# Kernel tuning notes

Hardware: AMD Instinct MI355X
Metric: run time of the kernel (lower is better)

The kernel has to match this reference:

```python
import jax, jax.numpy as jnp
import numpy as np

# torch grid_sample semantics: grid[...,0] indexes width, grid[...,1] height, grid[...,2] depth;
# align_corners=True -> idx = (g+1)/2*(size-1); padding_mode='zeros' -> out-of-range taps contribute 0.

def _bilinear(plane, gx, gy):
    # plane: (C,H,W); gx,gy: (P,) in [-1,1]. Returns (P,C).
    C, H, W = plane.shape
    ix = (gx + 1.0) * 0.5 * (W - 1)
    iy = (gy + 1.0) * 0.5 * (H - 1)
    x0 = jnp.floor(ix); y0 = jnp.floor(iy)
    wx = ix - x0; wy = iy - y0
    x0i = x0.astype(jnp.int32); x1i = x0i + 1
    y0i = y0.astype(jnp.int32); y1i = y0i + 1
    def tap(xi, yi):
        valid = ((xi >= 0) & (xi < W) & (yi >= 0) & (yi < H)).astype(plane.dtype)
        v = plane[:, jnp.clip(yi, 0, H - 1), jnp.clip(xi, 0, W - 1)]  # (C,P)
        return v * valid
    out = (tap(x0i, y0i) * ((1 - wx) * (1 - wy)) + tap(x1i, y0i) * (wx * (1 - wy))
         + tap(x0i, y1i) * ((1 - wx) * wy)      + tap(x1i, y1i) * (wx * wy))
    return out.T  # (P,C)


def _trilinear(vol, gx, gy, gz):
    # vol: (C,D,H,W); gx->W, gy->H, gz->D. Returns (P,C).
    C, D, H, W = vol.shape
    ix = (gx + 1.0) * 0.5 * (W - 1)
    iy = (gy + 1.0) * 0.5 * (H - 1)
    iz = (gz + 1.0) * 0.5 * (D - 1)
    x0 = jnp.floor(ix); y0 = jnp.floor(iy); z0 = jnp.floor(iz)
    wx = ix - x0; wy = iy - y0; wz = iz - z0
    x0i = x0.astype(jnp.int32); y0i = y0.astype(jnp.int32); z0i = z0.astype(jnp.int32)
    def tap(xi, yi, zi):
        valid = ((xi >= 0) & (xi < W) & (yi >= 0) & (yi < H) & (zi >= 0) & (zi < D)).astype(vol.dtype)
        v = vol[:, jnp.clip(zi, 0, D - 1), jnp.clip(yi, 0, H - 1), jnp.clip(xi, 0, W - 1)]
        return v * valid
    out = jnp.zeros((C, gx.shape[0]), vol.dtype)
    for dz, wz_ in ((0, 1 - wz), (1, wz)):
        for dy, wy_ in ((0, 1 - wy), (1, wy)):
            for dx, wx_ in ((0, 1 - wx), (1, wx)):
                out = out + tap(x0i + dx, y0i + dy, z0i + dz) * (wx_ * wy_ * wz_)
    return out.T


def setup_inputs() -> dict:
    key = jax.random.key(0)
    ks = jax.random.split(key, 16)
    P, Cp, Np_, Cl, Nl, Cv, Nv = 262144, 32, 128, 64, 128, 16, 64
    s = 0.001
    d = {
        'coordinates': jax.random.uniform(ks[0], (1, P, 3), jnp.float32, -1.0, 1.0),
        'plane_xy': jax.random.normal(ks[1], (Cp, Np_, Np_)) * s,
        'plane_yz': jax.random.normal(ks[2], (Cp, Np_, Np_)) * s,
        'plane_xz': jax.random.normal(ks[3], (Cp, Np_, Np_)) * s,
        'plane_xy_g': jax.random.normal(ks[4], (Cp, Np_, Np_)) * s,
        'plane_yz_g': jax.random.normal(ks[5], (Cp, Np_, Np_)) * s,
        'plane_xz_g': jax.random.normal(ks[6], (Cp, Np_, Np_)) * s,
        'line_x': jax.random.normal(ks[7], (Cl, Nl, 1)) * s,
        'line_y': jax.random.normal(ks[8], (Cl, Nl, 1)) * s,
        'line_z': jax.random.normal(ks[9], (Cl, Nl, 1)) * s,
        'line_x_g': jax.random.normal(ks[10], (Cl, Nl, 1)) * s,
        'line_y_g': jax.random.normal(ks[11], (Cl, Nl, 1)) * s,
        'line_z_g': jax.random.normal(ks[12], (Cl, Nl, 1)) * s,
        'volume': jax.random.normal(ks[13], (Cv, Nv, Nv, Nv)) * s,
        'volume_g': jax.random.normal(ks[14], (Cv, Nv, Nv, Nv)) * s,
    }
    return d


def reference(coordinates, plane_xy, plane_yz, plane_xz, plane_xy_g, plane_yz_g, plane_xz_g,
              line_x, line_y, line_z, line_x_g, line_y_g, line_z_g, volume, volume_g):
    c = coordinates[0]  # (P,3), batch squeezed as in torch .squeeze(0)
    x, y, z = c[:, 0], c[:, 1], c[:, 2]
    zero = jnp.zeros_like(x)
    # Planes: coords2d (a,b) -> grid x=a (width), grid y=b (height).
    xy_e = _bilinear(plane_xy, x, y); xy_g = _bilinear(plane_xy_g, x, y)
    yz_e = _bilinear(plane_yz, y, z); yz_g = _bilinear(plane_yz_g, y, z)
    xz_e = _bilinear(plane_xz, x, z); xz_g = _bilinear(plane_xz_g, x, z)
    feats = jnp.sum(xy_e * (xy_g >= 0) + yz_e * (yz_g >= 0) + xz_e * (xz_g >= 0), axis=-1)
    # Lines: grid pair is (coord, 0) -> coord indexes the singleton width dim (faithful to torch).
    x_e = _bilinear(line_x, x, zero); x_g = _bilinear(line_x_g, x, zero)
    y_e = _bilinear(line_y, y, zero); y_g = _bilinear(line_y_g, y, zero)
    z_e = _bilinear(line_z, z, zero); z_g = _bilinear(line_z_g, z, zero)
    line_feats = jnp.sum(x_e * (x_g >= 0) + y_e * (y_g >= 0) + z_e * (z_g >= 0), axis=-1)
    # Volume: grid (x,y,z) -> x:W, y:H, z:D.
    v_e = _trilinear(volume, x, y, z); v_g = _trilinear(volume_g, x, y, z)
    vol_feats = jnp.sum(v_e * (v_g >= 0), axis=-1)
    return feats + line_feats + vol_feats  # (P,)
```

## Files before the change

kernel.cpp:

```cpp
#include <hip/hip_runtime.h>
#include <hip/hip_bf16.h>

#pragma clang fp contract(off)

typedef unsigned short u16;
typedef unsigned int u32;
typedef __attribute__((ext_vector_type(4))) float f32x4;
typedef __attribute__((ext_vector_type(8))) unsigned short u16x8;
typedef __attribute__((ext_vector_type(4))) unsigned short u16x4;

__device__ __forceinline__ float bf2f(u16 u) {
    union { unsigned int i; float f; } v; v.i = ((unsigned int)u) << 16; return v.f;
}
__device__ __forceinline__ u16 f2bf(float f) {
    __hip_bfloat16 h = __float2bfloat16(f);
    return *(u16*)&h;
}

__device__ __forceinline__ int cell_of(float x, float y, float z)
{
    int cx = (int)fminf(fmaxf((x + 1.0f) * 4.0f, 0.0f), 7.0f);
    int cy = (int)fminf(fmaxf((y + 1.0f) * 4.0f, 0.0f), 7.0f);
    int cz = (int)fminf(fmaxf((z + 1.0f) * 4.0f, 0.0f), 7.0f);
    return cx + (cy << 3) + (cz << 6);
}

__global__ __launch_bounds__(256) void fused_prep_count(
    const float* __restrict__ pxy, const float* __restrict__ pxyg,
    const float* __restrict__ pyz, const float* __restrict__ pyzg,
    const float* __restrict__ pxz, const float* __restrict__ pxzg,
    const float* __restrict__ vol, const float* __restrict__ volg,
    char* __restrict__ tpxy, char* __restrict__ tpyz, char* __restrict__ tpxz,
    char* __restrict__ tv,
    const float* __restrict__ coords, u32* __restrict__ hist, int P)
{
    __shared__ float smem[4352];
    const int b = blockIdx.x;
    const int t = threadIdx.x;

    if (b < 768) {
        int which = b >> 8, blk = b & 255;
        const float* e = (which == 0) ? pxy  : (which == 1) ? pyz  : pxz;
        const float* g = (which == 0) ? pxyg : (which == 1) ? pyzg : pxzg;
        char* dst      = (which == 0) ? tpxy : (which == 1) ? tpyz : tpxz;
        const int tbase = blk * 64;
#pragma unroll
        for (int i = 0; i < 4; ++i) {
            int eidx = i * 256 + t;
            int c = eidx >> 4;
            int q = eidx & 15;
            const float* src = (c < 32) ? e : g;
            int cs = (c < 32) ? c : (c - 32);
            f32x4 v = *(const f32x4*)(src + (size_t)cs * 16384 + tbase + q * 4);
            *(f32x4*)&smem[c * 68 + q * 4] = v;
        }
        __syncthreads();
#pragma unroll
        for (int i = 0; i < 3; ++i) {
            int sid = i * 256 + t;
            int rec = sid / 12;
            int seg = sid % 12;
            char* outp = dst + (size_t)(tbase + rec) * 192 + seg * 16;
            if (seg < 4) {
                u16x8 pk;
#pragma unroll
                for (int k = 0; k < 8; ++k) pk[k] = f2bf(smem[(seg * 8 + k) * 68 + rec]);
                *(u16x8*)outp = pk;
            } else {
                f32x4 pk;
#pragma unroll
                for (int k = 0; k < 4; ++k) pk[k] = smem[(32 + (seg - 4) * 4 + k) * 68 + rec];
                *(f32x4*)outp = pk;
            }
        }
    } else if (b < 2816) {
        int blk = b - 768;
        const int tbase = blk * 128;
#pragma unroll
        for (int i = 0; i < 4; ++i) {
            int eidx = i * 256 + t;
            int c = eidx >> 5;
            int q = eidx & 31;
            const float* src = (c < 16) ? vol : volg;
            int cs = (c < 16) ? c : (c - 16);
            f32x4 v = *(const f32x4*)(src + (size_t)cs * 262144 + tbase + q * 4);
            *(f32x4*)&smem[c * 132 + q * 4] = v;
        }
        __syncthreads();
#pragma unroll
        for (int i = 0; i < 3; ++i) {
            int sid = i * 256 + t;
            int rec = sid / 6;
            int seg = sid % 6;
            char* outp = tv + (size_t)(tbase + rec) * 96 + seg * 16;
            if (seg < 2) {
                u16x8 pk;
#pragma unroll
                for (int k = 0; k < 8; ++k) pk[k] = f2bf(smem[(seg * 8 + k) * 132 + rec]);
                *(u16x8*)outp = pk;
            } else {
                f32x4 pk;
#pragma unroll
                for (int k = 0; k < 4; ++k) pk[k] = smem[(16 + (seg - 2) * 4 + k) * 132 + rec];
                *(f32x4*)outp = pk;
            }
        }
    } else {
        u32* h = (u32*)smem;
        int blk = b - 2816;
        h[t] = 0u; h[t + 256] = 0u;
        __syncthreads();
        int p = blk * 256 + t;
        if (p < P) {
            float x = coords[3 * p + 0];
            float y = coords[3 * p + 1];
            float z = coords[3 * p + 2];
            atomicAdd(&h[cell_of(x, y, z)], 1u);
        }
        __syncthreads();
        u32* hb = hist + (size_t)blk * 512;
        hb[t] = h[t];
        hb[t + 256] = h[t + 256];
    }
}

__global__ __launch_bounds__(256) void cell_base(
    const u32* __restrict__ hist, u32* __restrict__ base,
    u32* __restrict__ totals, int nb)
{
    int c = blockIdx.x;
    int t = threadIdx.x;
    int b0 = t * 4;
    u32 v[4];
#pragma unroll
    for (int i = 0; i < 4; ++i)
        v[i] = (b0 + i < nb) ? hist[(size_t)(b0 + i) * 512 + c] : 0u;
    u32 lsum = v[0] + v[1] + v[2] + v[3];
    __shared__ u32 ls[256];
    ls[t] = lsum;
    __syncthreads();
#pragma unroll
    for (int off = 1; off < 256; off <<= 1) {
        u32 x = (t >= off) ? ls[t - off] : 0u;
        __syncthreads();
        ls[t] += x;
        __syncthreads();
    }
    u32 acc = ls[t] - lsum;
#pragma unroll
    for (int i = 0; i < 4; ++i) {
        if (b0 + i < nb) base[(size_t)(b0 + i) * 512 + c] = acc;
        acc += v[i];
    }
    if (t == 255) totals[c] = acc;
}

__global__ __launch_bounds__(256) void bucket_scatter2(
    const float* __restrict__ coords, const u32* __restrict__ base,
    const u32* __restrict__ totals, u32* __restrict__ perm, int P)
{
    __shared__ u32 lh[512];
    __shared__ u32 ts[512];
    __shared__ u32 torig[512];
    int t = threadIdx.x;
    lh[t] = 0u; lh[t + 256] = 0u;
    u32 a0 = totals[t], a1 = totals[t + 256];
    ts[t] = a0; ts[t + 256] = a1;
    torig[t] = a0; torig[t + 256] = a1;
    __syncthreads();
#pragma unroll
    for (int off = 1; off < 512; off <<= 1) {
        u32 x0 = (t >= off) ? ts[t - off] : 0u;
        u32 x1 = (t + 256 >= off) ? ts[t + 256 - off] : 0u;
        __syncthreads();
        ts[t] += x0; ts[t + 256] += x1;
        __syncthreads();
    }
    ts[t]       -= torig[t];
    ts[t + 256] -= torig[t + 256];
    __syncthreads();

    int p = blockIdx.x * 256 + t;
    if (p < P) {
        float x = coords[3 * p + 0];
        float y = coords[3 * p + 1];
        float z = coords[3 * p + 2];
        int cell = cell_of(x, y, z);
        u32 rank = atomicAdd(&lh[cell], 1u);
        u32 pos = ts[cell] + base[(size_t)blockIdx.x * 512 + cell] + rank;
        perm[pos] = (u32)p;
    }
}

__device__ __forceinline__ float plane_lane(
    const char* __restrict__ tp, float gx, float gy, int s)
{
    float ix = fminf(fmaxf((gx + 1.0f) * 0.5f * 127.0f, 0.0f), 127.0f);
    float iy = fminf(fmaxf((gy + 1.0f) * 0.5f * 127.0f, 0.0f), 127.0f);
    float x0f = floorf(ix), y0f = floorf(iy);
    float wx = ix - x0f, wy = iy - y0f;
    int x0 = (int)x0f, y0 = (int)y0f;
    int x1 = x0 + 1, y1 = y0 + 1;
    float vx1 = (x1 < 128) ? 1.0f : 0.0f;
    float vy1 = (y1 < 128) ? 1.0f : 0.0f;
    int x1c = min(x1, 127), y1c = min(y1, 127);
    float omwx = 1.0f - wx, omwy = 1.0f - wy;
    float ws4[4];
    ws4[0] = omwx * omwy;
    ws4[1] = (wx * omwy) * vx1;
    ws4[2] = (omwx * wy) * vy1;
    ws4[3] = ((wx * wy) * vx1) * vy1;
    unsigned o[4];
    o[0] = (unsigned)(y0  * 128 + x0 ) * 192u;
    o[1] = (unsigned)(y0  * 128 + x1c) * 192u;
    o[2] = (unsigned)(y1c * 128 + x0 ) * 192u;
    o[3] = (unsigned)(y1c * 128 + x1c) * 192u;

    const int eoff = s * 16;
    const int goff = 64 + s * 32;
    f32x4 ea0 = {0.0f, 0.0f, 0.0f, 0.0f}, ea1 = {0.0f, 0.0f, 0.0f, 0.0f};
    f32x4 ga0 = {0.0f, 0.0f, 0.0f, 0.0f}, ga1 = {0.0f, 0.0f, 0.0f, 0.0f};
#pragma unroll
    for (int t = 0; t < 4; ++t) {
        const char* bp = tp + o[t];
        float w = ws4[t];
        u16x8 ev = *(const u16x8*)(bp + eoff);
        f32x4 g0 = *(const f32x4*)(bp + goff);
        f32x4 g1 = *(const f32x4*)(bp + goff + 16);
#pragma unroll
        for (int j = 0; j < 4; ++j) {
            ga0[j] = ga0[j] + g0[j] * w;
            ga1[j] = ga1[j] + g1[j] * w;
            ea0[j] = fmaf(bf2f(ev[j]), w, ea0[j]);
            ea1[j] = fmaf(bf2f(ev[j + 4]), w, ea1[j]);
        }
    }
    float acc = 0.0f;
#pragma unroll
    for (int j = 0; j < 4; ++j) {
        acc += (ga0[j] >= 0.0f) ? ea0[j] : 0.0f;
        acc += (ga1[j] >= 0.0f) ? ea1[j] : 0.0f;
    }
    return acc;
}

__device__ __forceinline__ float vol_lane(
    const char* __restrict__ tv, float gx, float gy, float gz, int s)
{
    float ix = fminf(fmaxf((gx + 1.0f) * 0.5f * 63.0f, 0.0f), 63.0f);
    float iy = fminf(fmaxf((gy + 1.0f) * 0.5f * 63.0f, 0.0f), 63.0f);
    float iz = fminf(fmaxf((gz + 1.0f) * 0.5f * 63.0f, 0.0f), 63.0f);
    float x0f = floorf(ix), y0f = floorf(iy), z0f = floorf(iz);
    float wx = ix - x0f, wy = iy - y0f, wz = iz - z0f;
    int x0 = (int)x0f, y0 = (int)y0f, z0 = (int)z0f;
    int x1 = x0 + 1, y1 = y0 + 1, z1 = z0 + 1;
    float fx[2] = {1.0f - wx, wx}, fy[2] = {1.0f - wy, wy}, fz[2] = {1.0f - wz, wz};
    float vx[2] = {1.0f, (x1 < 64) ? 1.0f : 0.0f};
    float vy[2] = {1.0f, (y1 < 64) ? 1.0f : 0.0f};
    float vz[2] = {1.0f, (z1 < 64) ? 1.0f : 0.0f};
    int xi[2] = {x0, min(x1, 63)}, yi[2] = {y0, min(y1, 63)}, zi[2] = {z0, min(z1, 63)};

    unsigned off[8];
    float w[8];
#pragma unroll
    for (int dz = 0; dz < 2; ++dz)
#pragma unroll
        for (int dy = 0; dy < 2; ++dy)
#pragma unroll
            for (int dx = 0; dx < 2; ++dx) {
                int tt = (dz << 2) | (dy << 1) | dx;
                w[tt] = (((fx[dx] * fy[dy]) * fz[dz]) * vx[dx]) * (vy[dy] * vz[dz]);
                off[tt] = (unsigned)((zi[dz] * 64 + yi[dy]) * 64 + xi[dx]) * 96u;
            }
    const int eoff = s * 8;
    const int goff = 32 + s * 16;
    f32x4 ea = {0.0f, 0.0f, 0.0f, 0.0f}, ga = {0.0f, 0.0f, 0.0f, 0.0f};
#pragma unroll
    for (int tt = 0; tt < 8; ++tt) {
        const char* bp = tv + off[tt];
        float wt = w[tt];
        u16x4 ev = *(const u16x4*)(bp + eoff);
        f32x4 gv = *(const f32x4*)(bp + goff);
#pragma unroll
        for (int j = 0; j < 4; ++j) {
            ga[j] = ga[j] + gv[j] * wt;
            ea[j] = fmaf(bf2f(ev[j]), wt, ea[j]);
        }
    }
    float acc = 0.0f;
#pragma unroll
    for (int j = 0; j < 4; ++j)
        acc += (ga[j] >= 0.0f) ? ea[j] : 0.0f;
    return acc;
}

__device__ __forceinline__ float line_pair(const float* __restrict__ e,
                                           const float* __restrict__ g, int c)
{
    float ev = e[c * 128 + 63] * 0.5f + e[c * 128 + 64] * 0.5f;
    float gv = g[c * 128 + 63] * 0.5f + g[c * 128 + 64] * 0.5f;
    return (gv >= 0.0f) ? ev : 0.0f;
}

__device__ __forceinline__ float block_line_const(
    const float* lx, const float* ly, const float* lz,
    const float* lxg, const float* lyg, const float* lzg)
{
    __shared__ float lc_sh;
    int t = threadIdx.x;
    if (t < 64) {
        float part = line_pair(lx, lxg, t) + line_pair(ly, lyg, t) + line_pair(lz, lzg, t);
#pragma unroll
        for (int off = 32; off > 0; off >>= 1) part += __shfl_down(part, off);
        if (t == 0) lc_sh = part;
    }
    __syncthreads();
    return lc_sh;
}

__global__ __launch_bounds__(256) void ctri_main_L2(
    const float* __restrict__ coords, const u32* __restrict__ perm,
    const float* __restrict__ lx,  const float* __restrict__ ly,  const float* __restrict__ lz,
    const float* __restrict__ lxg, const float* __restrict__ lyg, const float* __restrict__ lzg,
    const char* __restrict__ tpxy, const char* __restrict__ tpyz, const char* __restrict__ tpxz,
    const char* __restrict__ tv,
    float* __restrict__ out, int P, int nblk)
{
    float lc = block_line_const(lx, ly, lz, lxg, lyg, lzg);
    int b = blockIdx.x;
    int cpx = nblk >> 3;
    int swz = (b & 7) * cpx + (b >> 3);
    int g = threadIdx.x >> 2;
    int s = threadIdx.x & 3;
    int i0 = swz * 128 + g * 2;
    if (i0 >= P) return;
    int i1 = min(i0 + 1, P - 1);
    int p0 = (int)perm[i0];
    int p1 = (int)perm[i1];
    float x0 = coords[3 * p0 + 0], y0 = coords[3 * p0 + 1], z0 = coords[3 * p0 + 2];
    float x1 = coords[3 * p1 + 0], y1 = coords[3 * p1 + 1], z1 = coords[3 * p1 + 2];
    float a0 = 0.0f, a1 = 0.0f;
    a0 += plane_lane(tpxy, x0, y0, s);   a1 += plane_lane(tpxy, x1, y1, s);
    a0 += plane_lane(tpyz, y0, z0, s);   a1 += plane_lane(tpyz, y1, z1, s);
    a0 += plane_lane(tpxz, x0, z0, s);   a1 += plane_lane(tpxz, x1, z1, s);
    a0 += vol_lane(tv, x0, y0, z0, s);   a1 += vol_lane(tv, x1, y1, z1, s);
    a0 += __shfl_xor(a0, 1, 64);
    a0 += __shfl_xor(a0, 2, 64);
    a1 += __shfl_xor(a1, 1, 64);
    a1 += __shfl_xor(a1, 2, 64);
    if (s == 0) {
        out[p0] = lc + a0;
        if (i0 + 1 < P) out[p1] = lc + a1;
    }
}

__device__ __forceinline__ float sample_plane_pair_D(
    const float* __restrict__ e, const float* __restrict__ g, float gx, float gy)
{
    float ix = fminf(fmaxf((gx + 1.0f) * 0.5f * 127.0f, 0.0f), 127.0f);
    float iy = fminf(fmaxf((gy + 1.0f) * 0.5f * 127.0f, 0.0f), 127.0f);
    float x0f = floorf(ix), y0f = floorf(iy);
    float wx = ix - x0f, wy = iy - y0f;
    int x0 = (int)x0f, y0 = (int)y0f;
    int x1 = x0 + 1, y1 = y0 + 1;
    float vx1 = (x1 < 128) ? 1.0f : 0.0f;
    float vy1 = (y1 < 128) ? 1.0f : 0.0f;
    int x1c = min(x1, 127), y1c = min(y1, 127);
    float omwx = 1.0f - wx, omwy = 1.0f - wy;
    float w00 = omwx * omwy;
    float w10 = (wx * omwy) * vx1;
    float w01 = (omwx * wy) * vy1;
    float w11 = ((wx * wy) * vx1) * vy1;
    int o00 = y0 * 128 + x0, o10 = y0 * 128 + x1c;
    int o01 = y1c * 128 + x0, o11 = y1c * 128 + x1c;
    float acc = 0.0f;
#pragma unroll 4
    for (int c = 0; c < 32; ++c) {
        const float* ec = e + (size_t)c * 16384;
        const float* gc = g + (size_t)c * 16384;
        float ei = ((ec[o00] * w00 + ec[o10] * w10) + ec[o01] * w01) + ec[o11] * w11;
        float gi = ((gc[o00] * w00 + gc[o10] * w10) + gc[o01] * w01) + gc[o11] * w11;
        acc += (gi >= 0.0f) ? ei : 0.0f;
    }
    return acc;
}

__device__ __forceinline__ float sample_volume_D(
    const float* __restrict__ e, const float* __restrict__ g,
    float gx, float gy, float gz)
{
    float ix = fminf(fmaxf((gx + 1.0f) * 0.5f * 63.0f, 0.0f), 63.0f);
    float iy = fminf(fmaxf((gy + 1.0f) * 0.5f * 63.0f, 0.0f), 63.0f);
    float iz = fminf(fmaxf((gz + 1.0f) * 0.5f * 63.0f, 0.0f), 63.0f);
    float x0f = floorf(ix), y0f = floorf(iy), z0f = floorf(iz);
    float wx = ix - x0f, wy = iy - y0f, wz = iz - z0f;
    int x0 = (int)x0f, y0 = (int)y0f, z0 = (int)z0f;
    int x1 = x0 + 1, y1 = y0 + 1, z1 = z0 + 1;
    float fx[2] = {1.0f - wx, wx}, fy[2] = {1.0f - wy, wy}, fz[2] = {1.0f - wz, wz};
    float vx[2] = {1.0f, (x1 < 64) ? 1.0f : 0.0f};
    float vy[2] = {1.0f, (y1 < 64) ? 1.0f : 0.0f};
    float vz[2] = {1.0f, (z1 < 64) ? 1.0f : 0.0f};
    int xi[2] = {x0, min(x1, 63)}, yi[2] = {y0, min(y1, 63)}, zi[2] = {z0, min(z1, 63)};
    int o[8]; float w[8];
#pragma unroll
    for (int dz = 0; dz < 2; ++dz)
#pragma unroll
        for (int dy = 0; dy < 2; ++dy)
#pragma unroll
            for (int dx = 0; dx < 2; ++dx) {
                int tt = (dz << 2) | (dy << 1) | dx;
                w[tt] = (((fx[dx] * fy[dy]) * fz[dz]) * vx[dx]) * (vy[dy] * vz[dz]);
                o[tt] = (zi[dz] * 64 + yi[dy]) * 64 + xi[dx];
            }
    float acc = 0.0f;
#pragma unroll 2
    for (int c = 0; c < 16; ++c) {
        const float* ec = e + (size_t)c * 262144;
        const float* gc = g + (size_t)c * 262144;
        float ei = 0.0f, gi = 0.0f;
#pragma unroll
        for (int tt = 0; tt < 8; ++tt) {
            ei = ei + ec[o[tt]] * w[tt];
            gi = gi + gc[o[tt]] * w[tt];
        }
        acc += (gi >= 0.0f) ? ei : 0.0f;
    }
    return acc;
}

__global__ __launch_bounds__(256) void ctri_main_D(
    const float* __restrict__ coords,
    const float* __restrict__ lx,  const float* __restrict__ ly,  const float* __restrict__ lz,
    const float* __restrict__ lxg, const float* __restrict__ lyg, const float* __restrict__ lzg,
    const float* __restrict__ pxy, const float* __restrict__ pyz, const float* __restrict__ pxz,
    const float* __restrict__ pxyg, const float* __restrict__ pyzg, const float* __restrict__ pxzg,
    const float* __restrict__ vol, const float* __restrict__ volg,
    float* __restrict__ out, int P)
{
    float lc = block_line_const(lx, ly, lz, lxg, lyg, lzg);
    int p = blockIdx.x * blockDim.x + threadIdx.x;
    if (p >= P) return;
    float x = coords[3 * p + 0];
    float y = coords[3 * p + 1];
    float z = coords[3 * p + 2];
    float acc = lc;
    acc += sample_plane_pair_D(pxy, pxyg, x, y);
    acc += sample_plane_pair_D(pyz, pyzg, y, z);
    acc += sample_plane_pair_D(pxz, pxzg, x, z);
    acc += sample_volume_D(vol, volg, x, y, z);
    out[p] = acc;
}

extern "C" void kernel_launch(void* const* d_in, const int* in_sizes, int n_in,
                              void* d_out, int out_size, void* d_ws, size_t ws_size,
                              hipStream_t stream)
{
    (void)n_in; (void)out_size;
    const float* coords = (const float*)d_in[0];
    const float* pxy  = (const float*)d_in[1];
    const float* pyz  = (const float*)d_in[2];
    const float* pxz  = (const float*)d_in[3];
    const float* pxyg = (const float*)d_in[4];
    const float* pyzg = (const float*)d_in[5];
    const float* pxzg = (const float*)d_in[6];
    const float* lx   = (const float*)d_in[7];
    const float* ly   = (const float*)d_in[8];
    const float* lz   = (const float*)d_in[9];
    const float* lxg  = (const float*)d_in[10];
    const float* lyg  = (const float*)d_in[11];
    const float* lzg  = (const float*)d_in[12];
    const float* vol  = (const float*)d_in[13];
    const float* volg = (const float*)d_in[14];
    float* out = (float*)d_out;

    const int P = in_sizes[0] / 3;
    const int pblocks = (P + 255) / 256;
    const size_t planeRec = (size_t)16384 * 192;
    const size_t volRec   = (size_t)262144 * 96;
    const size_t tabBytes = 3 * planeRec + volRec;
    const size_t permBytes = (size_t)P * 4;
    const size_t histBytes = (size_t)pblocks * 512 * 4;
    const size_t need_bytes = tabBytes + permBytes + 2 * histBytes + 512 * 4;

    if (ws_size >= need_bytes) {
        char* tpxy = (char*)d_ws;
        char* tpyz = tpxy + planeRec;
        char* tpxz = tpyz + planeRec;
        char* tv   = tpxz + planeRec;
        u32* perm   = (u32*)(tv + volRec);
        u32* hist   = perm + P;
        u32* base   = hist + (size_t)pblocks * 512;
        u32* totals = base + (size_t)pblocks * 512;

        fused_prep_count<<<2816 + pblocks, 256, 0, stream>>>(
            pxy, pxyg, pyz, pyzg, pxz, pxzg, vol, volg,
            tpxy, tpyz, tpxz, tv, coords, hist, P);
        cell_base<<<512, 256, 0, stream>>>(hist, base, totals, pblocks);
        bucket_scatter2<<<pblocks, 256, 0, stream>>>(coords, base, totals, perm, P);

        const int mblocks = (P * 2 + 255) / 256;
        ctri_main_L2<<<mblocks, 256, 0, stream>>>(coords, perm, lx, ly, lz, lxg, lyg, lzg,
                                                  tpxy, tpyz, tpxz, tv, out, P, mblocks);
    } else {
        ctri_main_D<<<pblocks, 256, 0, stream>>>(coords, lx, ly, lz, lxg, lyg, lzg,
                                                 pxy, pyz, pxz, pxyg, pyzg, pxzg,
                                                 vol, volg, out, P);
    }
}
```

Baseline: 185.8 us.

## Scatter sorted coordinates directly and hoist line constant into cell_base

The scatter pass now writes packed (x,y,z,index) records in cell-sorted order instead of a permutation, so the main sampling kernel reads coordinates contiguously rather than gathering them through perm. Histogram and scatter blocks each handle 1024 points, which cuts the number of chunks and simplifies the per-cell scan to one entry per thread. The line-feature constant is computed once in cell_base and read from a buffer, instead of every main-kernel block recomputing it behind a __syncthreads. In exchange, sorted storage grows from 4 to 16 bytes per point, and each scatter block does more serial atomics.

Result: faster. 174.8 us (-5.9%).

```diff
diff --git a/kernel.cpp b/kernel.cpp
--- a/kernel.cpp
+++ b/kernel.cpp
@@ -110,12 +110,15 @@
         int blk = b - 2816;
         h[t] = 0u; h[t + 256] = 0u;
         __syncthreads();
-        int p = blk * 256 + t;
-        if (p < P) {
-            float x = coords[3 * p + 0];
-            float y = coords[3 * p + 1];
-            float z = coords[3 * p + 2];
-            atomicAdd(&h[cell_of(x, y, z)], 1u);
+#pragma unroll
+        for (int i = 0; i < 4; ++i) {
+            int p = blk * 1024 + i * 256 + t;
+            if (p < P) {
+                float x = coords[3 * p + 0];
+                float y = coords[3 * p + 1];
+                float z = coords[3 * p + 2];
+                atomicAdd(&h[cell_of(x, y, z)], 1u);
+            }
         }
         __syncthreads();
         u32* hb = hist + (size_t)blk * 512;
@@ -126,18 +129,16 @@
 
 __global__ __launch_bounds__(256) void cell_base(
     const u32* __restrict__ hist, u32* __restrict__ base,
-    u32* __restrict__ totals, int nb)
+    u32* __restrict__ totals, float* __restrict__ lcout,
+    const float* __restrict__ lx,  const float* __restrict__ ly,  const float* __restrict__ lz,
+    const float* __restrict__ lxg, const float* __restrict__ lyg, const float* __restrict__ lzg,
+    int nb)
 {
     int c = blockIdx.x;
     int t = threadIdx.x;
-    int b0 = t * 4;
-    u32 v[4];
-#pragma unroll
-    for (int i = 0; i < 4; ++i)
-        v[i] = (b0 + i < nb) ? hist[(size_t)(b0 + i) * 512 + c] : 0u;
-    u32 lsum = v[0] + v[1] + v[2] + v[3];
+    u32 v = (t < nb) ? hist[(size_t)t * 512 + c] : 0u;
     __shared__ u32 ls[256];
-    ls[t] = lsum;
+    ls[t] = v;
     __syncthreads();
 #pragma unroll
     for (int off = 1; off < 256; off <<= 1) {
@@ -146,18 +147,29 @@
         ls[t] += x;
         __syncthreads();
     }
-    u32 acc = ls[t] - lsum;
-#pragma unroll
-    for (int i = 0; i < 4; ++i) {
-        if (b0 + i < nb) base[(size_t)(b0 + i) * 512 + c] = acc;
-        acc += v[i];
-    }
-    if (t == 255) totals[c] = acc;
-}
-
-__global__ __launch_bounds__(256) void bucket_scatter2(
+    if (t < nb) base[(size_t)t * 512 + c] = ls[t] - v;
+    if (t == 255) totals[c] = ls[255];
+
+    if (c == 0 && t < 64) {
+        float ev, gv, part = 0.0f;
+        ev = lx[t * 128 + 63] * 0.5f + lx[t * 128 + 64] * 0.5f;
+        gv = lxg[t * 128 + 63] * 0.5f + lxg[t * 128 + 64] * 0.5f;
+        part += (gv >= 0.0f) ? ev : 0.0f;
+        ev = ly[t * 128 + 63] * 0.5f + ly[t * 128 + 64] * 0.5f;
+        gv = lyg[t * 128 + 63] * 0.5f + lyg[t * 128 + 64] * 0.5f;
+        part += (gv >= 0.0f) ? ev : 0.0f;
+        ev = lz[t * 128 + 63] * 0.5f + lz[t * 128 + 64] * 0.5f;
+        gv = lzg[t * 128 + 63] * 0.5f + lzg[t * 128 + 64] * 0.5f;
+        part += (gv >= 0.0f) ? ev : 0.0f;
+#pragma unroll
+        for (int off = 32; off > 0; off >>= 1) part += __shfl_down(part, off);
+        if (t == 0) lcout[0] = part;
+    }
+}
+
+__global__ __launch_bounds__(256) void scatter_sorted(
     const float* __restrict__ coords, const u32* __restrict__ base,
-    const u32* __restrict__ totals, u32* __restrict__ perm, int P)
+    const u32* __restrict__ totals, f32x4* __restrict__ sorted, int P)
 {
     __shared__ u32 lh[512];
     __shared__ u32 ts[512];
@@ -180,15 +192,20 @@
     ts[t + 256] -= torig[t + 256];
     __syncthreads();
 
-    int p = blockIdx.x * 256 + t;
-    if (p < P) {
-        float x = coords[3 * p + 0];
-        float y = coords[3 * p + 1];
-        float z = coords[3 * p + 2];
-        int cell = cell_of(x, y, z);
-        u32 rank = atomicAdd(&lh[cell], 1u);
-        u32 pos = ts[cell] + base[(size_t)blockIdx.x * 512 + cell] + rank;
-        perm[pos] = (u32)p;
+    int blk = blockIdx.x;
+#pragma unroll
+    for (int i = 0; i < 4; ++i) {
+        int p = blk * 1024 + i * 256 + t;
+        if (p < P) {
+            float x = coords[3 * p + 0];
+            float y = coords[3 * p + 1];
+            float z = coords[3 * p + 2];
+            int cell = cell_of(x, y, z);
+            u32 rank = atomicAdd(&lh[cell], 1u);
+            u32 pos = ts[cell] + base[(size_t)blk * 512 + cell] + rank;
+            f32x4 v = {x, y, z, __uint_as_float((u32)p)};
+            sorted[pos] = v;
+        }
     }
 }
 
@@ -294,39 +311,13 @@
     return acc;
 }
 
-__device__ __forceinline__ float line_pair(const float* __restrict__ e,
-                                           const float* __restrict__ g, int c)
-{
-    float ev = e[c * 128 + 63] * 0.5f + e[c * 128 + 64] * 0.5f;
-    float gv = g[c * 128 + 63] * 0.5f + g[c * 128 + 64] * 0.5f;
-    return (gv >= 0.0f) ? ev : 0.0f;
-}
-
-__device__ __forceinline__ float block_line_const(
-    const float* lx, const float* ly, const float* lz,
-    const float* lxg, const float* lyg, const float* lzg)
-{
-    __shared__ float lc_sh;
-    int t = threadIdx.x;
-    if (t < 64) {
-        float part = line_pair(lx, lxg, t) + line_pair(ly, lyg, t) + line_pair(lz, lzg, t);
-#pragma unroll
-        for (int off = 32; off > 0; off >>= 1) part += __shfl_down(part, off);
-        if (t == 0) lc_sh = part;
-    }
-    __syncthreads();
-    return lc_sh;
-}
-
-__global__ __launch_bounds__(256) void ctri_main_L2(
-    const float* __restrict__ coords, const u32* __restrict__ perm,
-    const float* __restrict__ lx,  const float* __restrict__ ly,  const float* __restrict__ lz,
-    const float* __restrict__ lxg, const float* __restrict__ lyg, const float* __restrict__ lzg,
+__global__ __launch_bounds__(256) void ctri_main_S2(
+    const f32x4* __restrict__ sorted, const float* __restrict__ lcbuf,
     const char* __restrict__ tpxy, const char* __restrict__ tpyz, const char* __restrict__ tpxz,
     const char* __restrict__ tv,
     float* __restrict__ out, int P, int nblk)
 {
-    float lc = block_line_const(lx, ly, lz, lxg, lyg, lzg);
+    float lc = lcbuf[0];
     int b = blockIdx.x;
     int cpx = nblk >> 3;
     int swz = (b & 7) * cpx + (b >> 3);
@@ -335,15 +326,15 @@
     int i0 = swz * 128 + g * 2;
     if (i0 >= P) return;
     int i1 = min(i0 + 1, P - 1);
-    int p0 = (int)perm[i0];
-    int p1 = (int)perm[i1];
-    float x0 = coords[3 * p0 + 0], y0 = coords[3 * p0 + 1], z0 = coords[3 * p0 + 2];
-    float x1 = coords[3 * p1 + 0], y1 = coords[3 * p1 + 1], z1 = coords[3 * p1 + 2];
+    f32x4 s0 = sorted[i0];
+    f32x4 s1 = sorted[i1];
+    int p0 = (int)__float_as_uint(s0[3]);
+    int p1 = (int)__float_as_uint(s1[3]);
     float a0 = 0.0f, a1 = 0.0f;
-    a0 += plane_lane(tpxy, x0, y0, s);   a1 += plane_lane(tpxy, x1, y1, s);
-    a0 += plane_lane(tpyz, y0, z0, s);   a1 += plane_lane(tpyz, y1, z1, s);
-    a0 += plane_lane(tpxz, x0, z0, s);   a1 += plane_lane(tpxz, x1, z1, s);
-    a0 += vol_lane(tv, x0, y0, z0, s);   a1 += vol_lane(tv, x1, y1, z1, s);
+    a0 += plane_lane(tpxy, s0[0], s0[1], s);    a1 += plane_lane(tpxy, s1[0], s1[1], s);
+    a0 += plane_lane(tpyz, s0[1], s0[2], s);    a1 += plane_lane(tpyz, s1[1], s1[2], s);
+    a0 += plane_lane(tpxz, s0[0], s0[2], s);    a1 += plane_lane(tpxz, s1[0], s1[2], s);
+    a0 += vol_lane(tv, s0[0], s0[1], s0[2], s); a1 += vol_lane(tv, s1[0], s1[1], s1[2], s);
     a0 += __shfl_xor(a0, 1, 64);
     a0 += __shfl_xor(a0, 2, 64);
     a1 += __shfl_xor(a1, 1, 64);
@@ -352,6 +343,30 @@
         out[p0] = lc + a0;
         if (i0 + 1 < P) out[p1] = lc + a1;
     }
+}
+
+__device__ __forceinline__ float line_pair(const float* __restrict__ e,
+                                           const float* __restrict__ g, int c)
+{
+    float ev = e[c * 128 + 63] * 0.5f + e[c * 128 + 64] * 0.5f;
+    float gv = g[c * 128 + 63] * 0.5f + g[c * 128 + 64] * 0.5f;
+    return (gv >= 0.0f) ? ev : 0.0f;
+}
+
+__device__ __forceinline__ float block_line_const(
+    const float* lx, const float* ly, const float* lz,
+    const float* lxg, const float* lyg, const float* lzg)
+{
+    __shared__ float lc_sh;
+    int t = threadIdx.x;
+    if (t < 64) {
+        float part = line_pair(lx, lxg, t) + line_pair(ly, lyg, t) + line_pair(lz, lzg, t);
+#pragma unroll
+        for (int off = 32; off > 0; off >>= 1) part += __shfl_down(part, off);
+        if (t == 0) lc_sh = part;
+    }
+    __syncthreads();
+    return lc_sh;
 }
 
 __device__ __forceinline__ float sample_plane_pair_D(
@@ -474,34 +489,37 @@
     float* out = (float*)d_out;
 
     const int P = in_sizes[0] / 3;
-    const int pblocks = (P + 255) / 256;
+    const int chunks = (P + 1023) / 1024;
     const size_t planeRec = (size_t)16384 * 192;
     const size_t volRec   = (size_t)262144 * 96;
     const size_t tabBytes = 3 * planeRec + volRec;
-    const size_t permBytes = (size_t)P * 4;
-    const size_t histBytes = (size_t)pblocks * 512 * 4;
-    const size_t need_bytes = tabBytes + permBytes + 2 * histBytes + 512 * 4;
+    const size_t sortBytes = (size_t)P * 16;
+    const size_t histBytes = (size_t)chunks * 512 * 4;
+    const size_t need_bytes = tabBytes + sortBytes + 2 * histBytes + 512 * 4 + 64;
 
     if (ws_size >= need_bytes) {
         char* tpxy = (char*)d_ws;
         char* tpyz = tpxy + planeRec;
         char* tpxz = tpyz + planeRec;
         char* tv   = tpxz + planeRec;
-        u32* perm   = (u32*)(tv + volRec);
-        u32* hist   = perm + P;
-        u32* base   = hist + (size_t)pblocks * 512;
-        u32* totals = base + (size_t)pblocks * 512;
-
-        fused_prep_count<<<2816 + pblocks, 256, 0, stream>>>(
+        f32x4* sorted = (f32x4*)(tv + volRec);
+        u32* hist   = (u32*)(sorted + P);
+        u32* base   = hist + (size_t)chunks * 512;
+        u32* totals = base + (size_t)chunks * 512;
+        float* lcbuf = (float*)(totals + 512);
+
+        fused_prep_count<<<2816 + chunks, 256, 0, stream>>>(
             pxy, pxyg, pyz, pyzg, pxz, pxzg, vol, volg,
             tpxy, tpyz, tpxz, tv, coords, hist, P);
-        cell_base<<<512, 256, 0, stream>>>(hist, base, totals, pblocks);
-        bucket_scatter2<<<pblocks, 256, 0, stream>>>(coords, base, totals, perm, P);
+        cell_base<<<512, 256, 0, stream>>>(hist, base, totals, lcbuf,
+                                           lx, ly, lz, lxg, lyg, lzg, chunks);
+        scatter_sorted<<<chunks, 256, 0, stream>>>(coords, base, totals, sorted, P);
 
         const int mblocks = (P * 2 + 255) / 256;
-        ctri_main_L2<<<mblocks, 256, 0, stream>>>(coords, perm, lx, ly, lz, lxg, lyg, lzg,
+        ctri_main_S2<<<mblocks, 256, 0, stream>>>(sorted, lcbuf,
                                                   tpxy, tpyz, tpxz, tv, out, P, mblocks);
     } else {
+        const int pblocks = (P + 255) / 256;
         ctri_main_D<<<pblocks, 256, 0, stream>>>(coords, lx, ly, lz, lxg, lyg, lzg,
                                                  pxy, pyz, pxz, pxyg, pyzg, pxzg,
                                                  vol, volg, out, P);
```
